# Optimization experiments

Measured on AMD Instinct MI355X. Metric: run time of the kernel, lower is better.

## Reference

```python
import jax, jax.numpy as jnp
import numpy as np

VOCAB = 50257
EXTRA = 64          # static over-approximation of num_oovs
SEQ = 1024
T_DEC = 100
E = 128
H = 160             # encoder hidden per direction; decoder hidden = 2H = 320
UNK = 3
START = 0
NEG = -1e9


def lstm_cell(x, h, c, wih, whh, bih, bhh):
    # torch gate order: i, f, g, o
    g = x @ wih.T + h @ whh.T + bih + bhh
    i, f, gg, o = jnp.split(g, 4, axis=-1)
    c = jax.nn.sigmoid(f) * c + jax.nn.sigmoid(i) * jnp.tanh(gg)
    h = jax.nn.sigmoid(o) * jnp.tanh(c)
    return h, c


def run_lstm(xs, wih, whh, bih, bhh, hdim):
    def step(carry, x):
        h, c = carry
        h, c = lstm_cell(x, h, c, wih, whh, bih, bhh)
        return (h, c), h
    init = (jnp.zeros((hdim,), xs.dtype), jnp.zeros((hdim,), xs.dtype))
    (hf, _), hs = jax.lax.scan(step, init, xs)
    return hs, hf


def setup_inputs() -> dict:
    key = jax.random.key(0)
    ks = jax.random.split(key, 20)
    rn = lambda k, shape, s: (jax.random.normal(k, shape, dtype=jnp.float32) * s)
    inp = {
        'input_ids': jax.random.randint(ks[0], (SEQ,), 0, VOCAB + EXTRA),
        'embedding': rn(ks[1], (VOCAB, E), 0.1),
        'enc_wih_f': rn(ks[2], (4 * H, E), 0.08),
        'enc_whh_f': rn(ks[3], (4 * H, H), 0.08),
        'enc_bih_f': rn(ks[4], (4 * H,), 0.05),
        'enc_bhh_f': rn(ks[5], (4 * H,), 0.05),
        'enc_wih_b': rn(ks[6], (4 * H, E), 0.08),
        'enc_whh_b': rn(ks[7], (4 * H, H), 0.08),
        'enc_bih_b': rn(ks[8], (4 * H,), 0.05),
        'enc_bhh_b': rn(ks[9], (4 * H,), 0.05),
        'dec_wih': rn(ks[10], (8 * H, E), 0.08),
        'dec_whh': rn(ks[11], (8 * H, 2 * H), 0.08),
        'dec_bih': rn(ks[12], (8 * H,), 0.05),
        'dec_bhh': rn(ks[13], (8 * H,), 0.05),
        'enc_attn_proj': rn(ks[14], (2 * H, 2 * H), 0.02),
        'dec_attn_proj': rn(ks[15], (2 * H, 2 * H), 0.02),
        'vocab_proj': rn(ks[16], (E, 6 * H), 0.05),
        'out_bias': rn(ks[17], (VOCAB,), 0.01),
        'switch_w': rn(ks[18], (1, 6 * H), 0.05),
        'switch_b': rn(ks[19], (1,), 0.05),
    }
    return inp


def reference(input_ids, embedding, enc_wih_f, enc_whh_f, enc_bih_f, enc_bhh_f,
              enc_wih_b, enc_whh_b, enc_bih_b, enc_bhh_b,
              dec_wih, dec_whh, dec_bih, dec_bhh,
              enc_attn_proj, dec_attn_proj, vocab_proj, out_bias,
              switch_w, switch_b):
    ids_in = jnp.where(input_ids >= VOCAB, UNK, input_ids)
    emb = embedding[ids_in]                               # [S, E]

    # bidirectional encoder LSTM
    h_fwd, hfin_f = run_lstm(emb, enc_wih_f, enc_whh_f, enc_bih_f, enc_bhh_f, H)
    h_bwd_rev, hfin_b = run_lstm(emb[::-1], enc_wih_b, enc_whh_b, enc_bih_b, enc_bhh_b, H)
    enc_h = jnp.concatenate([h_fwd, h_bwd_rev[::-1]], axis=-1)   # [S, 2H]

    # step-invariant vocab projection: tanh(W_emb @ vocab_proj) -> [V, 6H]
    out_proj = jnp.tanh(embedding @ vocab_proj)

    # precompute projected encoder states for attention: [S, 2H]
    enc_proj_h = enc_h @ enc_attn_proj.T

    h0 = jnp.concatenate([hfin_f, hfin_b])                # [2H]
    c0 = jnp.zeros((2 * H,), enc_h.dtype)
    dec_buf0 = jnp.zeros((T_DEC, 2 * H), enc_h.dtype)
    cum0 = jnp.zeros((SEQ,), enc_h.dtype)
    tok0 = jnp.asarray(START, dtype=input_ids.dtype)
    t_range = jnp.arange(T_DEC)

    def step(carry, t):
        h, c, cum, dec_buf, tok = carry
        x = embedding[jnp.where(tok >= VOCAB, UNK, tok)]
        h, c = lstm_cell(x, h, c, dec_wih, dec_whh, dec_bih, dec_bhh)

        # intra-temporal encoder attention
        scores = enc_proj_h @ h                           # [S] = h @ W_e @ enc_h.T
        cum_safe = jnp.where(t == 0, 1.0, cum)
        temporal = jnp.where(t == 0, scores, jnp.exp(scores) / cum_safe)
        attn = jax.nn.softmax(temporal)
        enc_ctx = attn @ enc_h                            # [2H]

        # intra-decoder attention over previous decoder hidden states
        dscores = (h @ dec_attn_proj) @ dec_buf.T         # [T_DEC]
        dmask = t_range < t
        dattn = jax.nn.softmax(jnp.where(dmask, dscores, NEG))
        dec_ctx = jnp.where(t == 0, jnp.zeros_like(h), dattn @ dec_buf)

        concat = jnp.concatenate([h, enc_ctx, dec_ctx])   # [6H]
        vocab_dist = jax.nn.softmax(out_proj @ concat + out_bias)  # [V]
        p_copy = jax.nn.sigmoid(jnp.dot(switch_w[0], concat) + switch_b[0])
        gen = jnp.pad((1.0 - p_copy) * vocab_dist, (0, EXTRA))     # [V+EXTRA]
        final = gen.at[input_ids].add(p_copy * attn)      # pointer scatter-add

        cum = cum + scores
        dec_buf = dec_buf.at[t].set(h)
        tok = jnp.argmax(final).astype(input_ids.dtype)   # greedy decode
        return (h, c, cum, dec_buf, tok), final

    _, finals = jax.lax.scan(step, (h0, c0, cum0, dec_buf0, tok0), t_range)
    return finals                                         # [T_DEC, V+EXTRA]
```

## Files before the change

### kernel.cpp

```cpp
#include <hip/hip_runtime.h>
#include <cstdint>

#define VOCAB 50257
#define VTOT  50321
#define TDEC  100
#define UNK   3
#define VPB   99

static const size_t OFF_EMB    = 0;
static const size_t OFF_WIHT_F = 131072;
static const size_t OFF_WIHT_B = 212992;
static const size_t OFF_WTE    = 294912;
static const size_t OFF_XG     = 397312;
static const size_t OFF_ENCH   = 1708032;
static const size_t OFF_EPH    = 2035712;
static const size_t OFF_DECBUF = 2363392;
static const size_t OFF_LOGITS = 2395392;
static const size_t OFF_SCORES = 2446080;
static const size_t OFF_GATES  = 2447104;
static const size_t OFF_HPAR   = 2448384;
static const size_t OFF_CPAR   = 2450944;
static const size_t OFF_DCTX   = 2456064;
static const size_t OFF_H      = 2456384;
static const size_t OFF_H0     = 2456704;
static const size_t OFF_CA     = 2457024;
static const size_t OFF_CB     = 2457344;
static const size_t OFF_CUMA   = 2457664;
static const size_t OFF_CUMB   = 2458688;
static const size_t OFF_ATTN   = 2459712;
static const size_t OFF_BM     = 2460736;
static const size_t OFF_BS     = 2461248;
static const size_t OFF_AVAL   = 2461760;
static const size_t OFF_AIDX   = 2462272;
static const size_t OFF_SCAL   = 2462784;
static const size_t OFF_SKEY   = 2462848;
static const size_t OFF_SPOS   = 2463872;
static const size_t OFF_BSTART = 2464896;
static const size_t OFF_WBF16  = 2465792;

__device__ __forceinline__ float sigmf(float x) { return 1.f / (1.f + expf(-x)); }

__device__ __forceinline__ float wsum64(float x) {
#pragma unroll
  for (int m = 1; m < 64; m <<= 1) x += __shfl_xor(x, m, 64);
  return x;
}

__device__ __forceinline__ unsigned short bf16r(float x) {
  uint32_t b = __float_as_uint(x);
  uint32_t r = (b + 0x7fffu + ((b >> 16) & 1u)) >> 16;
  return (unsigned short)r;
}

__global__ __launch_bounds__(256) void k_setup(float* __restrict__ ws, const int* __restrict__ ids,
                                               const float* __restrict__ embt, const float* __restrict__ ewf,
                                               const float* __restrict__ ewb, const float* __restrict__ eap) {
  int idx = blockIdx.x * 256 + threadIdx.x;
  if (idx < 131072) {
    int tt = idx >> 7, e = idx & 127;
    int id = ids[tt]; if (id >= VOCAB) id = UNK;
    ws[OFF_EMB + idx] = embt[(size_t)id * 128 + e];
  } else if (idx < 212992) {
    int i = idx - 131072;
    int k = i / 640, g = i - (i / 640) * 640;
    ws[OFF_WIHT_F + i] = ewf[(size_t)g * 128 + k];
  } else if (idx < 294912) {
    int i = idx - 212992;
    int k = i / 640, g = i - (i / 640) * 640;
    ws[OFF_WIHT_B + i] = ewb[(size_t)g * 128 + k];
  } else if (idx < 397312) {
    int i = idx - 294912;
    int k = i / 320, j = i - (i / 320) * 320;
    ws[OFF_WTE + i] = eap[(size_t)j * 320 + k];
  } else if (idx < 398656) {
    int i = idx - 397312;
    if (i < 320) ws[OFF_CA + i] = 0.f;
    else         ws[OFF_CUMA + (i - 320)] = 0.f;
  }
}

__global__ __launch_bounds__(256) void k_xg(float* __restrict__ ws,
                                            const float* __restrict__ bif, const float* __restrict__ bhf,
                                            const float* __restrict__ bib, const float* __restrict__ bhb) {
  int idx = blockIdx.x * 256 + threadIdx.x;
  int d = idx / 655360;
  int r = idx - d * 655360;
  int tt = r / 640, g = r - (r / 640) * 640;
  const float* wT = ws + (d ? OFF_WIHT_B : OFF_WIHT_F);
  const float* er = ws + OFF_EMB + (size_t)(d ? (1023 - tt) : tt) * 128;
  float acc = d ? (bib[g] + bhb[g]) : (bif[g] + bhf[g]);
#pragma unroll 4
  for (int k = 0; k < 128; ++k) acc += er[k] * wT[(size_t)k * 640 + g];
  ws[OFF_XG + idx] = acc;
}

__global__ __launch_bounds__(256) void k_outproj(const float* __restrict__ embt, const float* __restrict__ vp,
                                                 float* __restrict__ ws) {
  __shared__ float As[64][128];
  __shared__ float Bs[128][64];
  const int tid = threadIdx.x;
  const int v0 = blockIdx.x * 64, n0 = blockIdx.y * 64;
  for (int c = 0; c < 32; ++c) {
    int idx = c * 256 + tid;
    int m = idx >> 7, k = idx & 127;
    int v = v0 + m;
    As[m][k] = (v < VOCAB) ? embt[(size_t)v * 128 + k] : 0.f;
    int k2 = idx >> 6, n = idx & 63;
    Bs[k2][n] = vp[(size_t)k2 * 960 + n0 + n];
  }
  __syncthreads();
  const int mi = tid >> 4, ni = tid & 15;
  float acc[4][4] = {};
  for (int k = 0; k < 128; ++k) {
    float a0 = As[mi * 4 + 0][k], a1 = As[mi * 4 + 1][k], a2 = As[mi * 4 + 2][k], a3 = As[mi * 4 + 3][k];
    float4 b = *(const float4*)&Bs[k][ni * 4];
    acc[0][0] += a0 * b.x; acc[0][1] += a0 * b.y; acc[0][2] += a0 * b.z; acc[0][3] += a0 * b.w;
    acc[1][0] += a1 * b.x; acc[1][1] += a1 * b.y; acc[1][2] += a1 * b.z; acc[1][3] += a1 * b.w;
    acc[2][0] += a2 * b.x; acc[2][1] += a2 * b.y; acc[2][2] += a2 * b.z; acc[2][3] += a2 * b.w;
    acc[3][0] += a3 * b.x; acc[3][1] += a3 * b.y; acc[3][2] += a3 * b.z; acc[3][3] += a3 * b.w;
  }
  unsigned short* W = (unsigned short*)(ws + OFF_WBF16);
#pragma unroll
  for (int i = 0; i < 4; ++i) {
    int v = v0 + mi * 4 + i;
    if (v < VOCAB) {
      ushort4 pk;
      pk.x = bf16r(tanhf(acc[i][0]));
      pk.y = bf16r(tanhf(acc[i][1]));
      pk.z = bf16r(tanhf(acc[i][2]));
      pk.w = bf16r(tanhf(acc[i][3]));
      *(ushort4*)&W[(size_t)v * 960 + n0 + ni * 4] = pk;
    }
  }
}

__global__ __launch_bounds__(512) void k_encoder(float* __restrict__ ws, const float* __restrict__ whh_f,
                                                 const float* __restrict__ whh_b) {
  const int dir = blockIdx.x;
  const int tid = threadIdx.x;
  const float* whh = dir ? whh_b : whh_f;
  const float* xg = ws + OFF_XG + (size_t)dir * 655360;
  __shared__ float hbuf[160];
  __shared__ float part[4][640];
  const int q = tid & 127, kg = tid >> 7, ks = kg * 40;
  float w[5][40];
#pragma unroll
  for (int j = 0; j < 5; ++j)
#pragma unroll
    for (int i = 0; i < 40; ++i)
      w[j][i] = whh[(size_t)(5 * q + j) * 160 + ks + i];
  float cst = 0.f;
  if (tid < 160) hbuf[tid] = 0.f;
  __syncthreads();
  for (int t = 0; t < 1024; ++t) {
    float acc[5] = {0.f, 0.f, 0.f, 0.f, 0.f};
#pragma unroll
    for (int i4 = 0; i4 < 10; ++i4) {
      float4 h4 = *(const float4*)&hbuf[ks + i4 * 4];
#pragma unroll
      for (int j = 0; j < 5; ++j)
        acc[j] += w[j][i4 * 4 + 0] * h4.x + w[j][i4 * 4 + 1] * h4.y + w[j][i4 * 4 + 2] * h4.z + w[j][i4 * 4 + 3] * h4.w;
    }
#pragma unroll
    for (int j = 0; j < 5; ++j) part[kg][5 * q + j] = acc[j];
    __syncthreads();
    if (tid < 160) {
      float gi = xg[(size_t)t * 640 + tid];
      float gf = xg[(size_t)t * 640 + 160 + tid];
      float gg = xg[(size_t)t * 640 + 320 + tid];
      float go = xg[(size_t)t * 640 + 480 + tid];
#pragma unroll
      for (int k2 = 0; k2 < 4; ++k2) {
        gi += part[k2][tid]; gf += part[k2][160 + tid];
        gg += part[k2][320 + tid]; go += part[k2][480 + tid];
      }
      cst = sigmf(gf) * cst + sigmf(gi) * tanhf(gg);
      float hn = sigmf(go) * tanhf(cst);
      hbuf[tid] = hn;
      int trow = dir ? (1023 - t) : t;
      ws[OFF_ENCH + (size_t)trow * 320 + dir * 160 + tid] = hn;
    }
    __syncthreads();
  }
  if (tid < 160) ws[OFF_H0 + dir * 160 + tid] = hbuf[tid];
}

__global__ __launch_bounds__(256) void k_encproj(float* __restrict__ ws) {
  int idx = blockIdx.x * 256 + threadIdx.x;
  int s = idx / 320, j = idx - (idx / 320) * 320;
  const float* er = ws + OFF_ENCH + (size_t)s * 320;
  const float* wt = ws + OFF_WTE;
  float acc = 0.f;
#pragma unroll 4
  for (int k = 0; k < 320; ++k) acc += er[k] * wt[(size_t)k * 320 + j];
  ws[OFF_EPH + idx] = acc;
}

__global__ __launch_bounds__(512) void k_sort(float* __restrict__ ws, const int* __restrict__ ids) {
  __shared__ int sk[1024], sp[1024];
  const int tid = threadIdx.x;
  for (int j = tid; j < 1024; j += 512) { sk[j] = ids[j]; sp[j] = j; }
  if (tid < 320) ws[OFF_H + tid] = ws[OFF_H0 + tid];
  __syncthreads();
  for (int k = 2; k <= 1024; k <<= 1)
    for (int j = k >> 1; j > 0; j >>= 1) {
      for (int i = tid; i < 1024; i += 512) {
        int ixj = i ^ j;
        if (ixj > i) {
          bool up = ((i & k) == 0);
          int a = sk[i], b2 = sk[ixj];
          if (up ? (a > b2) : (a < b2)) {
            sk[i] = b2; sk[ixj] = a;
            int pa = sp[i]; sp[i] = sp[ixj]; sp[ixj] = pa;
          }
        }
      }
      __syncthreads();
    }
  int* BST = (int*)(ws + OFF_BSTART);
  int* SK = (int*)(ws + OFF_SKEY);
  int* SP = (int*)(ws + OFF_SPOS);
  for (int j = tid; j < 1024; j += 512) {
    SK[j] = sk[j]; SP[j] = sp[j];
    int o1 = sk[j] / VPB;
    int o0 = (j == 0) ? -1 : (sk[j - 1] / VPB);
    for (int o = o0 + 1; o <= o1; ++o) BST[o] = j;
  }
  if (tid == 0) {
    int olast = sk[1023] / VPB;
    for (int o = olast + 1; o <= 512; ++o) BST[o] = 1024;
  }
}

__global__ __launch_bounds__(256) void k_d1_gates(float* __restrict__ ws, const float* __restrict__ embt,
                                                  const float* __restrict__ dwih, const float* __restrict__ dwhh,
                                                  const float* __restrict__ dbih, const float* __restrict__ dbhh,
                                                  int t) {
  __shared__ float rv[256];
  __shared__ int ri[256];
  const int tid = threadIdx.x, bid = blockIdx.x;
  int token = 0;
  if (t > 0) {
    float v0 = ws[OFF_AVAL + tid], v1 = ws[OFF_AVAL + 256 + tid];
    int i0 = ((const int*)(ws + OFF_AIDX))[tid], i1 = ((const int*)(ws + OFF_AIDX))[256 + tid];
    if (v1 > v0 || (v1 == v0 && i1 < i0)) { v0 = v1; i0 = i1; }
    rv[tid] = v0; ri[tid] = i0;
    __syncthreads();
    for (int off = 128; off > 0; off >>= 1) {
      if (tid < off) {
        float b = rv[tid + off]; int bi = ri[tid + off];
        if (b > rv[tid] || (b == rv[tid] && bi < ri[tid])) { rv[tid] = b; ri[tid] = bi; }
      }
      __syncthreads();
    }
    token = ri[0];
  }
  int tokm = (token >= VOCAB) ? UNK : token;
  const int l = tid & 63, wv = tid >> 6;
  float xv0 = embt[(size_t)tokm * 128 + l];
  float xv1 = embt[(size_t)tokm * 128 + 64 + l];
  float hv[5];
#pragma unroll
  for (int c = 0; c < 5; ++c) hv[c] = ws[OFF_H + c * 64 + l];
  const int wg = bid * 4 + wv;
  for (int i = 0; i < 16; ++i) {
    const int r = wg * 16 + i;
    float acc = dwih[(size_t)r * 128 + l] * xv0 + dwih[(size_t)r * 128 + 64 + l] * xv1;
#pragma unroll
    for (int c = 0; c < 5; ++c) acc += dwhh[(size_t)r * 320 + c * 64 + l] * hv[c];
    acc = wsum64(acc);
    if (l == 0) ws[OFF_GATES + r] = acc + dbih[r] + dbhh[r];
  }
}

__global__ __launch_bounds__(512) void k_d2_hs(float* __restrict__ ws, const float* __restrict__ dap, int t) {
  __shared__ float hL[320];
  const int tid = threadIdx.x, bid = blockIdx.x;
  const int par = t & 1;
  const float* cin = ws + (par ? OFF_CB : OFF_CA);
  float* cout = ws + (par ? OFF_CA : OFF_CB);
  if (tid < 320) {
    float gi = ws[OFF_GATES + tid];
    float gf = ws[OFF_GATES + 320 + tid];
    float gg = ws[OFF_GATES + 640 + tid];
    float go = ws[OFF_GATES + 960 + tid];
    float c = sigmf(gf) * cin[tid] + sigmf(gi) * tanhf(gg);
    float hn = sigmf(go) * tanhf(c);
    hL[tid] = hn;
    if (bid == 0) {
      cout[tid] = c;
      ws[OFF_H + tid] = hn;
      ws[OFF_DECBUF + (size_t)t * 320 + tid] = hn;
    }
  }
  __syncthreads();
  if (bid < 32) {
    const int l = tid & 63, wv = tid >> 6;
    float hv[5];
#pragma unroll
    for (int c = 0; c < 5; ++c) hv[c] = hL[c * 64 + l];
#pragma unroll
    for (int i = 0; i < 4; ++i) {
      int s = bid * 32 + wv * 4 + i;
      const float* er = ws + OFF_EPH + (size_t)s * 320;
      float acc = 0.f;
#pragma unroll
      for (int c = 0; c < 5; ++c) acc += er[c * 64 + l] * hv[c];
      acc = wsum64(acc);
      if (l == 0) ws[OFF_SCORES + s] = acc;
    }
  } else if (tid < 320) {
    int q = bid - 32;
    float acc = 0.f;
#pragma unroll 8
    for (int ii = 0; ii < 40; ++ii) {
      int i = q * 40 + ii;
      acc += hL[i] * dap[(size_t)i * 320 + tid];
    }
    ws[OFF_HPAR + q * 320 + tid] = acc;
  }
}

__global__ __launch_bounds__(512) void k_d3_attn(float* __restrict__ ws, int t) {
  __shared__ float attnL[1024];
  __shared__ float redA[512];
  __shared__ float dsL[128];
  __shared__ float daL[128];
  __shared__ float hpL[320];
  const int tid = threadIdx.x, bid = blockIdx.x;
  const int par = t & 1;
  const float* cumin = ws + (par ? OFF_CUMB : OFF_CUMA);
  float* cumout = ws + (par ? OFF_CUMA : OFF_CUMB);

  if (bid < 16) {
    float s0 = ws[OFF_SCORES + tid];
    float s1 = ws[OFF_SCORES + 512 + tid];
    float t0 = (t == 0) ? s0 : expf(s0) / cumin[tid];
    float t1 = (t == 0) ? s1 : expf(s1) / cumin[512 + tid];
    redA[tid] = fmaxf(t0, t1);
    __syncthreads();
    for (int off = 256; off > 0; off >>= 1) { if (tid < off) redA[tid] = fmaxf(redA[tid], redA[tid + off]); __syncthreads(); }
    float mx = redA[0];
    __syncthreads();
    redA[tid] = expf(t0 - mx) + expf(t1 - mx);
    __syncthreads();
    for (int off = 256; off > 0; off >>= 1) { if (tid < off) redA[tid] += redA[tid + off]; __syncthreads(); }
    float Ssm = redA[0];
    __syncthreads();
    attnL[tid] = expf(t0 - mx) / Ssm;
    attnL[512 + tid] = expf(t1 - mx) / Ssm;
    __syncthreads();
    if (tid < 64) ws[OFF_ATTN + bid * 64 + tid] = attnL[bid * 64 + tid];
    if (tid < 320) {
      float acc = 0.f;
      const float* eh = ws + OFF_ENCH + (size_t)(bid * 64) * 320 + tid;
#pragma unroll 4
      for (int k2 = 0; k2 < 64; ++k2) acc += attnL[bid * 64 + k2] * eh[(size_t)k2 * 320];
      ws[OFF_CPAR + bid * 320 + tid] = acc;
    }
  } else {
    cumout[tid] = cumin[tid] + ws[OFF_SCORES + tid];
    cumout[512 + tid] = cumin[512 + tid] + ws[OFF_SCORES + 512 + tid];
    if (tid < 320) {
      float a = 0.f;
#pragma unroll
      for (int q = 0; q < 8; ++q) a += ws[OFF_HPAR + q * 320 + tid];
      hpL[tid] = a;
    }
    __syncthreads();
    const int l = tid & 63, wv = tid >> 6;
    float hpv[5];
#pragma unroll
    for (int c = 0; c < 5; ++c) hpv[c] = hpL[c * 64 + l];
#pragma unroll
    for (int k2 = 0; k2 < 13; ++k2) {
      int tp = wv + 8 * k2;
      if (tp < t) {
        float acc = 0.f;
#pragma unroll
        for (int c = 0; c < 5; ++c) acc += hpv[c] * ws[OFF_DECBUF + (size_t)tp * 320 + c * 64 + l];
        acc = wsum64(acc);
        if (l == 0) dsL[tp] = acc;
      }
    }
    __syncthreads();
    float dv = -1e30f;
    if (tid < 128) { dv = (tid < t) ? dsL[tid] : -1e30f; redA[tid] = dv; }
    __syncthreads();
    for (int off = 64; off > 0; off >>= 1) { if (tid < off) redA[tid] = fmaxf(redA[tid], redA[tid + off]); __syncthreads(); }
    float dmx = redA[0];
    __syncthreads();
    float de = (tid < 128) ? expf(dv - dmx) : 0.f;
    if (tid < 128) redA[tid] = de;
    __syncthreads();
    for (int off = 64; off > 0; off >>= 1) { if (tid < off) redA[tid] += redA[tid + off]; __syncthreads(); }
    float dS = redA[0];
    __syncthreads();
    if (tid < 128) daL[tid] = de / dS;
    __syncthreads();
    if (tid < 320) {
      float acc = 0.f;
      for (int tp = 0; tp < t; ++tp) acc += daL[tp] * ws[OFF_DECBUF + (size_t)tp * 320 + tid];
      ws[OFF_DCTX + tid] = acc;
    }
  }
}

__global__ __launch_bounds__(256) void k_d4_logits(float* __restrict__ ws, const float* __restrict__ ob,
                                                   const float* __restrict__ sw, const float* __restrict__ sb) {
  __shared__ float concatL[960];
  __shared__ float logitsL[128];
  __shared__ float rm[256], rs[256];
  const int tid = threadIdx.x, bid = blockIdx.x;
  for (int i = tid; i < 960; i += 256) {
    float v;
    if (i < 320) v = ws[OFF_H + i];
    else if (i < 640) {
      int j = i - 320;
      float a = 0.f;
#pragma unroll
      for (int p = 0; p < 16; ++p) a += ws[OFF_CPAR + p * 320 + j];
      v = a;
    } else v = ws[OFF_DCTX + (i - 640)];
    concatL[i] = v;
  }
  __syncthreads();
  const int l = tid & 63, wv = tid >> 6;
  if (bid == 0 && tid < 64) {
    float acc = 0.f;
#pragma unroll
    for (int c = 0; c < 15; ++c) acc += sw[c * 64 + l] * concatL[c * 64 + l];
    acc = wsum64(acc);
    if (l == 0) ws[OFF_SCAL] = 1.f / (1.f + expf(-(acc + sb[0])));
  }
  const unsigned* W = (const unsigned*)(ws + OFF_WBF16);
  const float2* cL2 = (const float2*)concatL;
  float cc0[7], cc1[7], ct0 = 0.f, ct1 = 0.f;
#pragma unroll
  for (int c = 0; c < 7; ++c) { float2 x = cL2[c * 64 + l]; cc0[c] = x.x; cc1[c] = x.y; }
  if (l < 32) { ct0 = concatL[896 + 2 * l]; ct1 = concatL[897 + 2 * l]; }
  const int vbase = bid * VPB;
  const int r0 = wv * 25, r1 = (wv * 25 + 25 < VPB) ? (wv * 25 + 25) : VPB;
  for (int r = r0; r < r1; r += 2) {
    int va = vbase + r, vb = va + 1;
    bool oka = (va < VOCAB);
    bool okb = (r + 1 < r1) && (vb < VOCAB);
    float acc0 = 0.f, acc1 = 0.f;
    const unsigned* rowa = W + (size_t)va * 480;
    const unsigned* rowb = W + (size_t)vb * 480;
    unsigned ua[7], ub[7], ta = 0, tb = 0;
    if (oka) {
#pragma unroll
      for (int c = 0; c < 7; ++c) ua[c] = rowa[c * 64 + l];
      if (l < 32) ta = rowa[448 + l];
    }
    if (okb) {
#pragma unroll
      for (int c = 0; c < 7; ++c) ub[c] = rowb[c * 64 + l];
      if (l < 32) tb = rowb[448 + l];
    }
    if (oka) {
#pragma unroll
      for (int c = 0; c < 7; ++c)
        acc0 += __uint_as_float(ua[c] << 16) * cc0[c] + __uint_as_float(ua[c] & 0xffff0000u) * cc1[c];
      if (l < 32) acc0 += __uint_as_float(ta << 16) * ct0 + __uint_as_float(ta & 0xffff0000u) * ct1;
    }
    if (okb) {
#pragma unroll
      for (int c = 0; c < 7; ++c)
        acc1 += __uint_as_float(ub[c] << 16) * cc0[c] + __uint_as_float(ub[c] & 0xffff0000u) * cc1[c];
      if (l < 32) acc1 += __uint_as_float(tb << 16) * ct0 + __uint_as_float(tb & 0xffff0000u) * ct1;
    }
    acc0 = wsum64(acc0);
    acc1 = wsum64(acc1);
    if (l == 0) {
      if (oka) { float lg = acc0 + ob[va]; logitsL[r] = lg; ws[OFF_LOGITS + va] = lg; }
      else logitsL[r] = -1e30f;
      if (r + 1 < r1) {
        if (okb) { float lg = acc1 + ob[vb]; logitsL[r + 1] = lg; ws[OFF_LOGITS + vb] = lg; }
        else logitsL[r + 1] = -1e30f;
      }
    }
  }
  __syncthreads();
  bool valid = (tid < VPB) && (logitsL[tid < VPB ? tid : 0] > -1e29f) && (tid < VPB);
  float m = -1e30f, s = 0.f;
  if (tid < VPB) {
    float lv = logitsL[tid];
    if (lv > -1e29f) { m = lv; s = 1.f; }
  }
  (void)valid;
  rm[tid] = m; rs[tid] = s;
  __syncthreads();
  for (int off = 128; off > 0; off >>= 1) {
    if (tid < off) {
      float m1 = rm[tid], m2 = rm[tid + off];
      float mm = fmaxf(m1, m2);
      rs[tid] = rs[tid] * expf(m1 - mm) + rs[tid + off] * expf(m2 - mm);
      rm[tid] = mm;
    }
    __syncthreads();
  }
  if (tid == 0) { ws[OFF_BM + bid] = rm[0]; ws[OFF_BS + bid] = rs[0]; }
}

__global__ __launch_bounds__(128) void k_d5_final(float* __restrict__ ws, float* __restrict__ out, int t) {
  __shared__ float rm[128], rs[128];
  __shared__ float rv[128];
  __shared__ int ri[128];
  const int tid = threadIdx.x, bid = blockIdx.x;
  float m = -1e30f, s = 0.f;
#pragma unroll
  for (int k = 0; k < 4; ++k) {
    float m2 = ws[OFF_BM + tid * 4 + k], s2 = ws[OFF_BS + tid * 4 + k];
    float mm = fmaxf(m, m2);
    s = s * expf(m - mm) + s2 * expf(m2 - mm);
    m = mm;
  }
  rm[tid] = m; rs[tid] = s;
  __syncthreads();
  for (int off = 64; off > 0; off >>= 1) {
    if (tid < off) {
      float m1 = rm[tid], m2 = rm[tid + off];
      float mm = fmaxf(m1, m2);
      rs[tid] = rs[tid] * expf(m1 - mm) + rs[tid + off] * expf(m2 - mm);
      rm[tid] = mm;
    }
    __syncthreads();
  }
  float M = rm[0], Sg = rs[0];
  float pc = ws[OFF_SCAL];
  float scale = (1.f - pc) / Sg;
  const int* BST = (const int*)(ws + OFF_BSTART);
  const int* SK = (const int*)(ws + OFF_SKEY);
  const int* SP = (const int*)(ws + OFF_SPOS);
  int v = bid * VPB + tid;
  bool act = (tid < VPB) && (v < VTOT);
  float val = -1e30f;
  if (act) {
    val = (v < VOCAB) ? scale * expf(ws[OFF_LOGITS + v] - M) : 0.f;
    int jb = BST[bid], je = BST[bid + 1];
    for (int j = jb; j < je; ++j)
      if (SK[j] == v) val += pc * ws[OFF_ATTN + SP[j]];
    out[(size_t)t * VTOT + v] = val;
  }
  rv[tid] = act ? val : -1e30f; ri[tid] = v;
  __syncthreads();
  for (int off = 64; off > 0; off >>= 1) {
    if (tid < off) {
      float v2 = rv[tid + off]; int i2 = ri[tid + off];
      if (v2 > rv[tid] || (v2 == rv[tid] && i2 < ri[tid])) { rv[tid] = v2; ri[tid] = i2; }
    }
    __syncthreads();
  }
  if (tid == 0) { ws[OFF_AVAL + bid] = rv[0]; ((int*)(ws + OFF_AIDX))[bid] = ri[0]; }
}

extern "C" void kernel_launch(void* const* d_in, const int* in_sizes, int n_in,
                              void* d_out, int out_size, void* d_ws, size_t ws_size,
                              hipStream_t stream) {
  const int*   ids  = (const int*)d_in[0];
  const float* embt = (const float*)d_in[1];
  const float* ewf  = (const float*)d_in[2];
  const float* ehf  = (const float*)d_in[3];
  const float* ebif = (const float*)d_in[4];
  const float* ebhf = (const float*)d_in[5];
  const float* ewb  = (const float*)d_in[6];
  const float* ehb  = (const float*)d_in[7];
  const float* ebib = (const float*)d_in[8];
  const float* ebhb = (const float*)d_in[9];
  const float* dwih = (const float*)d_in[10];
  const float* dwhh = (const float*)d_in[11];
  const float* dbih = (const float*)d_in[12];
  const float* dbhh = (const float*)d_in[13];
  const float* eap  = (const float*)d_in[14];
  const float* dap  = (const float*)d_in[15];
  const float* vp   = (const float*)d_in[16];
  const float* ob   = (const float*)d_in[17];
  const float* sw   = (const float*)d_in[18];
  const float* sb   = (const float*)d_in[19];
  float* out = (float*)d_out;
  float* ws  = (float*)d_ws;

  k_setup<<<1558, 256, 0, stream>>>(ws, ids, embt, ewf, ewb, eap);
  k_xg<<<5120, 256, 0, stream>>>(ws, ebif, ebhf, ebib, ebhb);
  k_outproj<<<dim3(786, 15), 256, 0, stream>>>(embt, vp, ws);
  k_encoder<<<2, 512, 0, stream>>>(ws, ehf, ehb);
  k_encproj<<<1280, 256, 0, stream>>>(ws);
  k_sort<<<1, 512, 0, stream>>>(ws, ids);

  for (int t = 0; t < TDEC; ++t) {
    k_d1_gates<<<20, 256, 0, stream>>>(ws, embt, dwih, dwhh, dbih, dbhh, t);
    k_d2_hs<<<40, 512, 0, stream>>>(ws, dap, t);
    k_d3_attn<<<17, 512, 0, stream>>>(ws, t);
    k_d4_logits<<<512, 256, 0, stream>>>(ws, ob, sw, sb);
    k_d5_final<<<512, 128, 0, stream>>>(ws, out, t);
  }
}
```

Measured before the change: 7.863 ms.

## Fuse per-step decoder kernels into one persistent kernel with grid barriers

```diff
diff --git a/kernel.cpp b/kernel.cpp
--- a/kernel.cpp
+++ b/kernel.cpp
@@ -5,7 +5,9 @@
 #define VTOT  50321
 #define TDEC  100
 #define UNK   3
-#define VPB   99
+#define NBLK  256
+#define NTHR  512
+#define VPB   198
 
 static const size_t OFF_EMB    = 0;
 static const size_t OFF_WIHT_F = 131072;
@@ -38,6 +40,10 @@
 static const size_t OFF_BSTART = 2464896;
 static const size_t OFF_WBF16  = 2465792;
 
+static const size_t OFF_PMS  = OFF_LOGITS;
+static const size_t OFF_TEMP = OFF_SCORES;
+static const size_t OFF_BAR  = OFF_SCAL;
+
 __device__ __forceinline__ float sigmf(float x) { return 1.f / (1.f + expf(-x)); }
 
 __device__ __forceinline__ float wsum64(float x) {
@@ -50,6 +56,25 @@
   uint32_t b = __float_as_uint(x);
   uint32_t r = (b + 0x7fffu + ((b >> 16) & 1u)) >> 16;
   return (unsigned short)r;
+}
+
+__device__ __forceinline__ void gridbar(float* ws) {
+  int* bar = (int*)(ws + OFF_BAR);
+  __syncthreads();
+  if (threadIdx.x == 0) {
+    __threadfence();
+    int g = __hip_atomic_load(&bar[1], __ATOMIC_RELAXED, __HIP_MEMORY_SCOPE_AGENT);
+    int old = __hip_atomic_fetch_add(&bar[0], 1, __ATOMIC_ACQ_REL, __HIP_MEMORY_SCOPE_AGENT);
+    if (old == NBLK - 1) {
+      __hip_atomic_store(&bar[0], 0, __ATOMIC_RELAXED, __HIP_MEMORY_SCOPE_AGENT);
+      __hip_atomic_store(&bar[1], g + 1, __ATOMIC_RELEASE, __HIP_MEMORY_SCOPE_AGENT);
+    } else {
+      while (__hip_atomic_load(&bar[1], __ATOMIC_RELAXED, __HIP_MEMORY_SCOPE_AGENT) == g)
+        __builtin_amdgcn_s_sleep(2);
+    }
+    __threadfence();
+  }
+  __syncthreads();
 }
 
 __global__ __launch_bounds__(256) void k_setup(float* __restrict__ ws, const int* __restrict__ ids,
@@ -72,10 +97,6 @@
     int i = idx - 294912;
     int k = i / 320, j = i - (i / 320) * 320;
     ws[OFF_WTE + i] = eap[(size_t)j * 320 + k];
-  } else if (idx < 398656) {
-    int i = idx - 397312;
-    if (i < 320) ws[OFF_CA + i] = 0.f;
-    else         ws[OFF_CUMA + (i - 320)] = 0.f;
   }
 }
 
@@ -200,7 +221,6 @@
   __shared__ int sk[1024], sp[1024];
   const int tid = threadIdx.x;
   for (int j = tid; j < 1024; j += 512) { sk[j] = ids[j]; sp[j] = j; }
-  if (tid < 320) ws[OFF_H + tid] = ws[OFF_H0 + tid];
   __syncthreads();
   for (int k = 2; k <= 1024; k <<= 1)
     for (int j = k >> 1; j > 0; j >>= 1) {
@@ -228,332 +248,306 @@
   }
   if (tid == 0) {
     int olast = sk[1023] / VPB;
-    for (int o = olast + 1; o <= 512; ++o) BST[o] = 1024;
-  }
-}
-
-__global__ __launch_bounds__(256) void k_d1_gates(float* __restrict__ ws, const float* __restrict__ embt,
-                                                  const float* __restrict__ dwih, const float* __restrict__ dwhh,
-                                                  const float* __restrict__ dbih, const float* __restrict__ dbhh,
-                                                  int t) {
-  __shared__ float rv[256];
-  __shared__ int ri[256];
-  const int tid = threadIdx.x, bid = blockIdx.x;
-  int token = 0;
-  if (t > 0) {
-    float v0 = ws[OFF_AVAL + tid], v1 = ws[OFF_AVAL + 256 + tid];
-    int i0 = ((const int*)(ws + OFF_AIDX))[tid], i1 = ((const int*)(ws + OFF_AIDX))[256 + tid];
-    if (v1 > v0 || (v1 == v0 && i1 < i0)) { v0 = v1; i0 = i1; }
-    rv[tid] = v0; ri[tid] = i0;
+    for (int o = olast + 1; o <= NBLK; ++o) BST[o] = 1024;
+    int* bar = (int*)(ws + OFF_BAR);
+    bar[0] = 0; bar[1] = 0;
+  }
+}
+
+__global__ __launch_bounds__(512) void k_decode(float* __restrict__ ws, float* __restrict__ out,
+    const float* __restrict__ embt,
+    const float* __restrict__ dwih, const float* __restrict__ dwhh,
+    const float* __restrict__ dbih, const float* __restrict__ dbhh,
+    const float* __restrict__ dap, const float* __restrict__ sw,
+    const float* __restrict__ sb, const float* __restrict__ ob) {
+  const int b = blockIdx.x, tid = threadIdx.x;
+  const int l = tid & 63, w = tid >> 6;
+  __shared__ float hL[320], cL[320];
+  __shared__ __align__(16) float concatL[960];
+  __shared__ float logitsL[VPB];
+  __shared__ float tauL[4], cumL[4];
+  __shared__ float redA[512], redB[512];
+  __shared__ int   redI[512];
+  __shared__ float attnL[64], dsL[128], daL[128], hpL[320];
+  __shared__ float pcS;
+
+  if (tid < 320) { hL[tid] = ws[OFF_H0 + tid]; cL[tid] = 0.f; }
+  if (tid < 4) cumL[tid] = 0.f;
+  __syncthreads();
+
+  for (int t = 0; t < TDEC; ++t) {
+    int token = 0;
+    if (t > 0) {
+      float av = -1e30f; int ai = 0;
+      if (tid < 256) { av = ws[OFF_AVAL + tid]; ai = ((const int*)(ws + OFF_AIDX))[tid]; }
+      redA[tid] = av; redI[tid] = ai;
+      __syncthreads();
+      for (int off = 256; off > 0; off >>= 1) {
+        if (tid < off) {
+          float v2 = redA[tid + off]; int i2 = redI[tid + off];
+          if (v2 > redA[tid] || (v2 == redA[tid] && i2 < redI[tid])) { redA[tid] = v2; redI[tid] = i2; }
+        }
+        __syncthreads();
+      }
+      token = redI[0];
+    }
+    int tokm = (token >= VOCAB) ? UNK : token;
+    if (w < 5) {
+      const int r = 5 * b + w;
+      float acc = dwih[(size_t)r * 128 + l] * embt[(size_t)tokm * 128 + l]
+                + dwih[(size_t)r * 128 + 64 + l] * embt[(size_t)tokm * 128 + 64 + l];
+#pragma unroll
+      for (int c = 0; c < 5; ++c) acc += dwhh[(size_t)r * 320 + c * 64 + l] * hL[c * 64 + l];
+      acc = wsum64(acc);
+      if (l == 0) ws[OFF_GATES + r] = acc + dbih[r] + dbhh[r];
+    }
+    gridbar(ws);
+
+    if (tid < 320) {
+      float gi = ws[OFF_GATES + tid];
+      float gf = ws[OFF_GATES + 320 + tid];
+      float gg = ws[OFF_GATES + 640 + tid];
+      float go = ws[OFF_GATES + 960 + tid];
+      float c = sigmf(gf) * cL[tid] + sigmf(gi) * tanhf(gg);
+      cL[tid] = c;
+      float hn = sigmf(go) * tanhf(c);
+      hL[tid] = hn;
+      if (b == 17) ws[OFF_DECBUF + (size_t)t * 320 + tid] = hn;
+    }
     __syncthreads();
-    for (int off = 128; off > 0; off >>= 1) {
-      if (tid < off) {
-        float b = rv[tid + off]; int bi = ri[tid + off];
-        if (b > rv[tid] || (b == rv[tid] && bi < ri[tid])) { rv[tid] = b; ri[tid] = bi; }
-      }
-      __syncthreads();
-    }
-    token = ri[0];
-  }
-  int tokm = (token >= VOCAB) ? UNK : token;
-  const int l = tid & 63, wv = tid >> 6;
-  float xv0 = embt[(size_t)tokm * 128 + l];
-  float xv1 = embt[(size_t)tokm * 128 + 64 + l];
-  float hv[5];
-#pragma unroll
-  for (int c = 0; c < 5; ++c) hv[c] = ws[OFF_H + c * 64 + l];
-  const int wg = bid * 4 + wv;
-  for (int i = 0; i < 16; ++i) {
-    const int r = wg * 16 + i;
-    float acc = dwih[(size_t)r * 128 + l] * xv0 + dwih[(size_t)r * 128 + 64 + l] * xv1;
-#pragma unroll
-    for (int c = 0; c < 5; ++c) acc += dwhh[(size_t)r * 320 + c * 64 + l] * hv[c];
-    acc = wsum64(acc);
-    if (l == 0) ws[OFF_GATES + r] = acc + dbih[r] + dbhh[r];
-  }
-}
-
-__global__ __launch_bounds__(512) void k_d2_hs(float* __restrict__ ws, const float* __restrict__ dap, int t) {
-  __shared__ float hL[320];
-  const int tid = threadIdx.x, bid = blockIdx.x;
-  const int par = t & 1;
-  const float* cin = ws + (par ? OFF_CB : OFF_CA);
-  float* cout = ws + (par ? OFF_CA : OFF_CB);
-  if (tid < 320) {
-    float gi = ws[OFF_GATES + tid];
-    float gf = ws[OFF_GATES + 320 + tid];
-    float gg = ws[OFF_GATES + 640 + tid];
-    float go = ws[OFF_GATES + 960 + tid];
-    float c = sigmf(gf) * cin[tid] + sigmf(gi) * tanhf(gg);
-    float hn = sigmf(go) * tanhf(c);
-    hL[tid] = hn;
-    if (bid == 0) {
-      cout[tid] = c;
-      ws[OFF_H + tid] = hn;
-      ws[OFF_DECBUF + (size_t)t * 320 + tid] = hn;
-    }
-  }
-  __syncthreads();
-  if (bid < 32) {
-    const int l = tid & 63, wv = tid >> 6;
-    float hv[5];
-#pragma unroll
-    for (int c = 0; c < 5; ++c) hv[c] = hL[c * 64 + l];
-#pragma unroll
-    for (int i = 0; i < 4; ++i) {
-      int s = bid * 32 + wv * 4 + i;
-      const float* er = ws + OFF_EPH + (size_t)s * 320;
+    if (w < 4) {
+      const int srow = 4 * b + w;
+      const float* er = ws + OFF_EPH + (size_t)srow * 320;
       float acc = 0.f;
 #pragma unroll
-      for (int c = 0; c < 5; ++c) acc += er[c * 64 + l] * hv[c];
+      for (int c = 0; c < 5; ++c) acc += er[c * 64 + l] * hL[c * 64 + l];
       acc = wsum64(acc);
-      if (l == 0) ws[OFF_SCORES + s] = acc;
-    }
-  } else if (tid < 320) {
-    int q = bid - 32;
-    float acc = 0.f;
+      float tau = (t == 0) ? acc : expf(acc) / cumL[w];
+      if (l == 0) {
+        tauL[w] = tau;
+        ws[OFF_TEMP + srow] = tau;
+        cumL[w] += acc;
+      }
+    }
+    if (b < 8 && tid < 320) {
+      float acc = 0.f;
 #pragma unroll 8
-    for (int ii = 0; ii < 40; ++ii) {
-      int i = q * 40 + ii;
-      acc += hL[i] * dap[(size_t)i * 320 + tid];
-    }
-    ws[OFF_HPAR + q * 320 + tid] = acc;
-  }
-}
-
-__global__ __launch_bounds__(512) void k_d3_attn(float* __restrict__ ws, int t) {
-  __shared__ float attnL[1024];
-  __shared__ float redA[512];
-  __shared__ float dsL[128];
-  __shared__ float daL[128];
-  __shared__ float hpL[320];
-  const int tid = threadIdx.x, bid = blockIdx.x;
-  const int par = t & 1;
-  const float* cumin = ws + (par ? OFF_CUMB : OFF_CUMA);
-  float* cumout = ws + (par ? OFF_CUMA : OFF_CUMB);
-
-  if (bid < 16) {
-    float s0 = ws[OFF_SCORES + tid];
-    float s1 = ws[OFF_SCORES + 512 + tid];
-    float t0 = (t == 0) ? s0 : expf(s0) / cumin[tid];
-    float t1 = (t == 0) ? s1 : expf(s1) / cumin[512 + tid];
-    redA[tid] = fmaxf(t0, t1);
+      for (int ii = 0; ii < 40; ++ii) {
+        int i = b * 40 + ii;
+        acc += hL[i] * dap[(size_t)i * 320 + tid];
+      }
+      ws[OFF_HPAR + b * 320 + tid] = acc;
+    }
     __syncthreads();
-    for (int off = 256; off > 0; off >>= 1) { if (tid < off) redA[tid] = fmaxf(redA[tid], redA[tid + off]); __syncthreads(); }
-    float mx = redA[0];
+    if (tid == 0) {
+      float m4 = fmaxf(fmaxf(tauL[0], tauL[1]), fmaxf(tauL[2], tauL[3]));
+      float s4 = expf(tauL[0] - m4) + expf(tauL[1] - m4) + expf(tauL[2] - m4) + expf(tauL[3] - m4);
+      ws[OFF_PMS + 2 * b] = m4;
+      ws[OFF_PMS + 2 * b + 1] = s4;
+    }
+    gridbar(ws);
+
+    if (b < 16) {
+      float m = -1e30f, s = 0.f;
+      if (tid < 256) { m = ws[OFF_PMS + 2 * tid]; s = ws[OFF_PMS + 2 * tid + 1]; }
+      redA[tid] = m; redB[tid] = s;
+      __syncthreads();
+      for (int off = 256; off > 0; off >>= 1) {
+        if (tid < off) {
+          float m1 = redA[tid], m2 = redA[tid + off];
+          float mx = fmaxf(m1, m2);
+          redB[tid] = redB[tid] * expf(m1 - mx) + redB[tid + off] * expf(m2 - mx);
+          redA[tid] = mx;
+        }
+        __syncthreads();
+      }
+      const float M = redA[0], S = redB[0];
+      __syncthreads();
+      if (tid < 64) {
+        float a = expf(ws[OFF_TEMP + 64 * b + tid] - M) / S;
+        attnL[tid] = a;
+        ws[OFF_ATTN + 64 * b + tid] = a;
+      }
+      __syncthreads();
+      if (tid < 320) {
+        float acc = 0.f;
+        const float* eh = ws + OFF_ENCH + (size_t)(64 * b) * 320 + tid;
+#pragma unroll 4
+        for (int k2 = 0; k2 < 64; ++k2) acc += attnL[k2] * eh[(size_t)k2 * 320];
+        ws[OFF_CPAR + b * 320 + tid] = acc;
+      }
+    } else if (b == 16) {
+      if (tid < 320) {
+        float a = 0.f;
+#pragma unroll
+        for (int q = 0; q < 8; ++q) a += ws[OFF_HPAR + q * 320 + tid];
+        hpL[tid] = a;
+      }
+      __syncthreads();
+      float hpv[5];
+#pragma unroll
+      for (int c = 0; c < 5; ++c) hpv[c] = hpL[c * 64 + l];
+#pragma unroll
+      for (int k2 = 0; k2 < 13; ++k2) {
+        int tp = w + 8 * k2;
+        if (tp < t) {
+          float acc = 0.f;
+#pragma unroll
+          for (int c = 0; c < 5; ++c) acc += hpv[c] * ws[OFF_DECBUF + (size_t)tp * 320 + c * 64 + l];
+          acc = wsum64(acc);
+          if (l == 0) dsL[tp] = acc;
+        }
+      }
+      __syncthreads();
+      float dv = -1e30f;
+      if (tid < 128) { dv = (tid < t) ? dsL[tid] : -1e30f; redA[tid] = dv; }
+      __syncthreads();
+      for (int off = 64; off > 0; off >>= 1) { if (tid < off) redA[tid] = fmaxf(redA[tid], redA[tid + off]); __syncthreads(); }
+      float dmx = redA[0];
+      __syncthreads();
+      float de = (tid < 128) ? expf(dv - dmx) : 0.f;
+      if (tid < 128) redA[tid] = de;
+      __syncthreads();
+      for (int off = 64; off > 0; off >>= 1) { if (tid < off) redA[tid] += redA[tid + off]; __syncthreads(); }
+      float dS = redA[0];
+      __syncthreads();
+      if (tid < 128) daL[tid] = de / dS;
+      __syncthreads();
+      if (tid < 320) {
+        float acc = 0.f;
+        for (int tp = 0; tp < t; ++tp) acc += daL[tp] * ws[OFF_DECBUF + (size_t)tp * 320 + tid];
+        ws[OFF_DCTX + tid] = (t == 0) ? 0.f : acc;
+      }
+    }
+    gridbar(ws);
+
+    if (tid < 320) {
+      float e = 0.f;
+#pragma unroll
+      for (int g2 = 0; g2 < 16; ++g2) e += ws[OFF_CPAR + g2 * 320 + tid];
+      concatL[tid] = hL[tid];
+      concatL[320 + tid] = e;
+      concatL[640 + tid] = ws[OFF_DCTX + tid];
+    }
     __syncthreads();
-    redA[tid] = expf(t0 - mx) + expf(t1 - mx);
+    if (w == 0) {
+      float acc = 0.f;
+#pragma unroll
+      for (int c = 0; c < 15; ++c) acc += sw[c * 64 + l] * concatL[c * 64 + l];
+      acc = wsum64(acc);
+      if (l == 0) pcS = 1.f / (1.f + expf(-(acc + sb[0])));
+    }
+    {
+      const unsigned* W = (const unsigned*)(ws + OFF_WBF16);
+      const float2* cL2 = (const float2*)concatL;
+      float cc0[7], cc1[7], ct0 = 0.f, ct1 = 0.f;
+#pragma unroll
+      for (int c = 0; c < 7; ++c) { float2 x = cL2[c * 64 + l]; cc0[c] = x.x; cc1[c] = x.y; }
+      if (l < 32) { ct0 = concatL[896 + 2 * l]; ct1 = concatL[897 + 2 * l]; }
+      const int vbase = b * VPB;
+      const int r0 = w * 25, r1 = (w * 25 + 25 < VPB) ? (w * 25 + 25) : VPB;
+      for (int r = r0; r < r1; r += 2) {
+        int va = vbase + r, vb2 = va + 1;
+        bool oka = (va < VOCAB);
+        bool okb = (r + 1 < r1) && (vb2 < VOCAB);
+        float acc0 = 0.f, acc1 = 0.f;
+        const unsigned* rowa = W + (size_t)va * 480;
+        const unsigned* rowb = W + (size_t)vb2 * 480;
+        unsigned ua[7], ub[7], ta = 0, tb = 0;
+        if (oka) {
+#pragma unroll
+          for (int c = 0; c < 7; ++c) ua[c] = rowa[c * 64 + l];
+          if (l < 32) ta = rowa[448 + l];
+        }
+        if (okb) {
+#pragma unroll
+          for (int c = 0; c < 7; ++c) ub[c] = rowb[c * 64 + l];
+          if (l < 32) tb = rowb[448 + l];
+        }
+        if (oka) {
+#pragma unroll
+          for (int c = 0; c < 7; ++c)
+            acc0 += __uint_as_float(ua[c] << 16) * cc0[c] + __uint_as_float(ua[c] & 0xffff0000u) * cc1[c];
+          if (l < 32) acc0 += __uint_as_float(ta << 16) * ct0 + __uint_as_float(ta & 0xffff0000u) * ct1;
+        }
+        if (okb) {
+#pragma unroll
+          for (int c = 0; c < 7; ++c)
+            acc1 += __uint_as_float(ub[c] << 16) * cc0[c] + __uint_as_float(ub[c] & 0xffff0000u) * cc1[c];
+          if (l < 32) acc1 += __uint_as_float(tb << 16) * ct0 + __uint_as_float(tb & 0xffff0000u) * ct1;
+        }
+        acc0 = wsum64(acc0);
+        acc1 = wsum64(acc1);
+        if (l == 0) {
+          logitsL[r] = oka ? (acc0 + ob[va]) : -1e30f;
+          if (r + 1 < r1) logitsL[r + 1] = okb ? (acc1 + ob[vb2]) : -1e30f;
+        }
+      }
+    }
     __syncthreads();
-    for (int off = 256; off > 0; off >>= 1) { if (tid < off) redA[tid] += redA[tid + off]; __syncthreads(); }
-    float Ssm = redA[0];
-    __syncthreads();
-    attnL[tid] = expf(t0 - mx) / Ssm;
-    attnL[512 + tid] = expf(t1 - mx) / Ssm;
-    __syncthreads();
-    if (tid < 64) ws[OFF_ATTN + bid * 64 + tid] = attnL[bid * 64 + tid];
-    if (tid < 320) {
-      float acc = 0.f;
-      const float* eh = ws + OFF_ENCH + (size_t)(bid * 64) * 320 + tid;
-#pragma unroll 4
-      for (int k2 = 0; k2 < 64; ++k2) acc += attnL[bid * 64 + k2] * eh[(size_t)k2 * 320];
-      ws[OFF_CPAR + bid * 320 + tid] = acc;
-    }
-  } else {
-    cumout[tid] = cumin[tid] + ws[OFF_SCORES + tid];
-    cumout[512 + tid] = cumin[512 + tid] + ws[OFF_SCORES + 512 + tid];
-    if (tid < 320) {
-      float a = 0.f;
-#pragma unroll
-      for (int q = 0; q < 8; ++q) a += ws[OFF_HPAR + q * 320 + tid];
-      hpL[tid] = a;
-    }
-    __syncthreads();
-    const int l = tid & 63, wv = tid >> 6;
-    float hpv[5];
-#pragma unroll
-    for (int c = 0; c < 5; ++c) hpv[c] = hpL[c * 64 + l];
-#pragma unroll
-    for (int k2 = 0; k2 < 13; ++k2) {
-      int tp = wv + 8 * k2;
-      if (tp < t) {
-        float acc = 0.f;
-#pragma unroll
-        for (int c = 0; c < 5; ++c) acc += hpv[c] * ws[OFF_DECBUF + (size_t)tp * 320 + c * 64 + l];
-        acc = wsum64(acc);
-        if (l == 0) dsL[tp] = acc;
-      }
-    }
-    __syncthreads();
-    float dv = -1e30f;
-    if (tid < 128) { dv = (tid < t) ? dsL[tid] : -1e30f; redA[tid] = dv; }
-    __syncthreads();
-    for (int off = 64; off > 0; off >>= 1) { if (tid < off) redA[tid] = fmaxf(redA[tid], redA[tid + off]); __syncthreads(); }
-    float dmx = redA[0];
-    __syncthreads();
-    float de = (tid < 128) ? expf(dv - dmx) : 0.f;
-    if (tid < 128) redA[tid] = de;
-    __syncthreads();
-    for (int off = 64; off > 0; off >>= 1) { if (tid < off) redA[tid] += redA[tid + off]; __syncthreads(); }
-    float dS = redA[0];
-    __syncthreads();
-    if (tid < 128) daL[tid] = de / dS;
-    __syncthreads();
-    if (tid < 320) {
-      float acc = 0.f;
-      for (int tp = 0; tp < t; ++tp) acc += daL[tp] * ws[OFF_DECBUF + (size_t)tp * 320 + tid];
-      ws[OFF_DCTX + tid] = acc;
-    }
-  }
-}
-
-__global__ __launch_bounds__(256) void k_d4_logits(float* __restrict__ ws, const float* __restrict__ ob,
-                                                   const float* __restrict__ sw, const float* __restrict__ sb) {
-  __shared__ float concatL[960];
-  __shared__ float logitsL[128];
-  __shared__ float rm[256], rs[256];
-  const int tid = threadIdx.x, bid = blockIdx.x;
-  for (int i = tid; i < 960; i += 256) {
-    float v;
-    if (i < 320) v = ws[OFF_H + i];
-    else if (i < 640) {
-      int j = i - 320;
-      float a = 0.f;
-#pragma unroll
-      for (int p = 0; p < 16; ++p) a += ws[OFF_CPAR + p * 320 + j];
-      v = a;
-    } else v = ws[OFF_DCTX + (i - 640)];
-    concatL[i] = v;
-  }
-  __syncthreads();
-  const int l = tid & 63, wv = tid >> 6;
-  if (bid == 0 && tid < 64) {
-    float acc = 0.f;
-#pragma unroll
-    for (int c = 0; c < 15; ++c) acc += sw[c * 64 + l] * concatL[c * 64 + l];
-    acc = wsum64(acc);
-    if (l == 0) ws[OFF_SCAL] = 1.f / (1.f + expf(-(acc + sb[0])));
-  }
-  const unsigned* W = (const unsigned*)(ws + OFF_WBF16);
-  const float2* cL2 = (const float2*)concatL;
-  float cc0[7], cc1[7], ct0 = 0.f, ct1 = 0.f;
-#pragma unroll
-  for (int c = 0; c < 7; ++c) { float2 x = cL2[c * 64 + l]; cc0[c] = x.x; cc1[c] = x.y; }
-  if (l < 32) { ct0 = concatL[896 + 2 * l]; ct1 = concatL[897 + 2 * l]; }
-  const int vbase = bid * VPB;
-  const int r0 = wv * 25, r1 = (wv * 25 + 25 < VPB) ? (wv * 25 + 25) : VPB;
-  for (int r = r0; r < r1; r += 2) {
-    int va = vbase + r, vb = va + 1;
-    bool oka = (va < VOCAB);
-    bool okb = (r + 1 < r1) && (vb < VOCAB);
-    float acc0 = 0.f, acc1 = 0.f;
-    const unsigned* rowa = W + (size_t)va * 480;
-    const unsigned* rowb = W + (size_t)vb * 480;
-    unsigned ua[7], ub[7], ta = 0, tb = 0;
-    if (oka) {
-#pragma unroll
-      for (int c = 0; c < 7; ++c) ua[c] = rowa[c * 64 + l];
-      if (l < 32) ta = rowa[448 + l];
-    }
-    if (okb) {
-#pragma unroll
-      for (int c = 0; c < 7; ++c) ub[c] = rowb[c * 64 + l];
-      if (l < 32) tb = rowb[448 + l];
-    }
-    if (oka) {
-#pragma unroll
-      for (int c = 0; c < 7; ++c)
-        acc0 += __uint_as_float(ua[c] << 16) * cc0[c] + __uint_as_float(ua[c] & 0xffff0000u) * cc1[c];
-      if (l < 32) acc0 += __uint_as_float(ta << 16) * ct0 + __uint_as_float(ta & 0xffff0000u) * ct1;
-    }
-    if (okb) {
-#pragma unroll
-      for (int c = 0; c < 7; ++c)
-        acc1 += __uint_as_float(ub[c] << 16) * cc0[c] + __uint_as_float(ub[c] & 0xffff0000u) * cc1[c];
-      if (l < 32) acc1 += __uint_as_float(tb << 16) * ct0 + __uint_as_float(tb & 0xffff0000u) * ct1;
-    }
-    acc0 = wsum64(acc0);
-    acc1 = wsum64(acc1);
-    if (l == 0) {
-      if (oka) { float lg = acc0 + ob[va]; logitsL[r] = lg; ws[OFF_LOGITS + va] = lg; }
-      else logitsL[r] = -1e30f;
-      if (r + 1 < r1) {
-        if (okb) { float lg = acc1 + ob[vb]; logitsL[r + 1] = lg; ws[OFF_LOGITS + vb] = lg; }
-        else logitsL[r + 1] = -1e30f;
-      }
-    }
-  }
-  __syncthreads();
-  bool valid = (tid < VPB) && (logitsL[tid < VPB ? tid : 0] > -1e29f) && (tid < VPB);
-  float m = -1e30f, s = 0.f;
-  if (tid < VPB) {
-    float lv = logitsL[tid];
-    if (lv > -1e29f) { m = lv; s = 1.f; }
-  }
-  (void)valid;
-  rm[tid] = m; rs[tid] = s;
-  __syncthreads();
-  for (int off = 128; off > 0; off >>= 1) {
-    if (tid < off) {
-      float m1 = rm[tid], m2 = rm[tid + off];
-      float mm = fmaxf(m1, m2);
-      rs[tid] = rs[tid] * expf(m1 - mm) + rs[tid + off] * expf(m2 - mm);
-      rm[tid] = mm;
-    }
-    __syncthreads();
-  }
-  if (tid == 0) { ws[OFF_BM + bid] = rm[0]; ws[OFF_BS + bid] = rs[0]; }
-}
-
-__global__ __launch_bounds__(128) void k_d5_final(float* __restrict__ ws, float* __restrict__ out, int t) {
-  __shared__ float rm[128], rs[128];
-  __shared__ float rv[128];
-  __shared__ int ri[128];
-  const int tid = threadIdx.x, bid = blockIdx.x;
-  float m = -1e30f, s = 0.f;
-#pragma unroll
-  for (int k = 0; k < 4; ++k) {
-    float m2 = ws[OFF_BM + tid * 4 + k], s2 = ws[OFF_BS + tid * 4 + k];
-    float mm = fmaxf(m, m2);
-    s = s * expf(m - mm) + s2 * expf(m2 - mm);
-    m = mm;
-  }
-  rm[tid] = m; rs[tid] = s;
-  __syncthreads();
-  for (int off = 64; off > 0; off >>= 1) {
-    if (tid < off) {
-      float m1 = rm[tid], m2 = rm[tid + off];
-      float mm = fmaxf(m1, m2);
-      rs[tid] = rs[tid] * expf(m1 - mm) + rs[tid + off] * expf(m2 - mm);
-      rm[tid] = mm;
-    }
-    __syncthreads();
-  }
-  float M = rm[0], Sg = rs[0];
-  float pc = ws[OFF_SCAL];
-  float scale = (1.f - pc) / Sg;
-  const int* BST = (const int*)(ws + OFF_BSTART);
-  const int* SK = (const int*)(ws + OFF_SKEY);
-  const int* SP = (const int*)(ws + OFF_SPOS);
-  int v = bid * VPB + tid;
-  bool act = (tid < VPB) && (v < VTOT);
-  float val = -1e30f;
-  if (act) {
-    val = (v < VOCAB) ? scale * expf(ws[OFF_LOGITS + v] - M) : 0.f;
-    int jb = BST[bid], je = BST[bid + 1];
-    for (int j = jb; j < je; ++j)
-      if (SK[j] == v) val += pc * ws[OFF_ATTN + SP[j]];
-    out[(size_t)t * VTOT + v] = val;
-  }
-  rv[tid] = act ? val : -1e30f; ri[tid] = v;
-  __syncthreads();
-  for (int off = 64; off > 0; off >>= 1) {
-    if (tid < off) {
-      float v2 = rv[tid + off]; int i2 = ri[tid + off];
-      if (v2 > rv[tid] || (v2 == rv[tid] && i2 < ri[tid])) { rv[tid] = v2; ri[tid] = i2; }
-    }
-    __syncthreads();
-  }
-  if (tid == 0) { ws[OFF_AVAL + bid] = rv[0]; ((int*)(ws + OFF_AIDX))[bid] = ri[0]; }
+    {
+      float m = -1e30f, s = 0.f;
+      if (tid < VPB) { float lv = logitsL[tid]; if (lv > -1e29f) { m = lv; s = 1.f; } }
+      redA[tid] = m; redB[tid] = s;
+      __syncthreads();
+      for (int off = 256; off > 0; off >>= 1) {
+        if (tid < off) {
+          float m1 = redA[tid], m2 = redA[tid + off];
+          float mx = fmaxf(m1, m2);
+          redB[tid] = redB[tid] * expf(m1 - mx) + redB[tid + off] * expf(m2 - mx);
+          redA[tid] = mx;
+        }
+        __syncthreads();
+      }
+      if (tid == 0) { ws[OFF_BM + b] = redA[0]; ws[OFF_BS + b] = redB[0]; }
+    }
+    gridbar(ws);
+
+    {
+      float m = -1e30f, s = 0.f;
+      if (tid < 256) { m = ws[OFF_BM + tid]; s = ws[OFF_BS + tid]; }
+      redA[tid] = m; redB[tid] = s;
+      __syncthreads();
+      for (int off = 256; off > 0; off >>= 1) {
+        if (tid < off) {
+          float m1 = redA[tid], m2 = redA[tid + off];
+          float mx = fmaxf(m1, m2);
+          redB[tid] = redB[tid] * expf(m1 - mx) + redB[tid + off] * expf(m2 - mx);
+          redA[tid] = mx;
+        }
+        __syncthreads();
+      }
+      const float M = redA[0], Sg = redB[0];
+      const float pc = pcS;
+      const float scale = (1.f - pc) / Sg;
+      __syncthreads();
+      const int* BST = (const int*)(ws + OFF_BSTART);
+      const int* SK = (const int*)(ws + OFF_SKEY);
+      const int* SP = (const int*)(ws + OFF_SPOS);
+      const int vbase = b * VPB;
+      int v = vbase + tid;
+      bool act = (tid < VPB) && (v < VTOT);
+      float val = -1e30f;
+      if (act) {
+        val = (v < VOCAB) ? scale * expf(logitsL[tid] - M) : 0.f;
+        int jb = BST[b], je = BST[b + 1];
+        for (int j = jb; j < je; ++j)
+          if (SK[j] == v) val += pc * ws[OFF_ATTN + SP[j]];
+        out[(size_t)t * VTOT + v] = val;
+      }
+      redA[tid] = act ? val : -1e30f; redI[tid] = v;
+      __syncthreads();
+      for (int off = 256; off > 0; off >>= 1) {
+        if (tid < off) {
+          float v2 = redA[tid + off]; int i2 = redI[tid + off];
+          if (v2 > redA[tid] || (v2 == redA[tid] && i2 < redI[tid])) { redA[tid] = v2; redI[tid] = i2; }
+        }
+        __syncthreads();
+      }
+      if (tid == 0) { ws[OFF_AVAL + b] = redA[0]; ((int*)(ws + OFF_AIDX))[b] = redI[0]; }
+    }
+    gridbar(ws);
+  }
 }
 
 extern "C" void kernel_launch(void* const* d_in, const int* in_sizes, int n_in,
@@ -588,12 +582,5 @@
   k_encoder<<<2, 512, 0, stream>>>(ws, ehf, ehb);
   k_encproj<<<1280, 256, 0, stream>>>(ws);
   k_sort<<<1, 512, 0, stream>>>(ws, ids);
-
-  for (int t = 0; t < TDEC; ++t) {
-    k_d1_gates<<<20, 256, 0, stream>>>(ws, embt, dwih, dwhh, dbih, dbhh, t);
-    k_d2_hs<<<40, 512, 0, stream>>>(ws, dap, t);
-    k_d3_attn<<<17, 512, 0, stream>>>(ws, t);
-    k_d4_logits<<<512, 256, 0, stream>>>(ws, ob, sw, sb);
-    k_d5_final<<<512, 128, 0, stream>>>(ws, out, t);
-  }
-}
+  k_decode<<<NBLK, NTHR, 0, stream>>>(ws, out, embt, dwih, dwhh, dbih, dbhh, dap, sw, sb, ob);
+}
```

Result: slower. 17.10 ms (+117.4%).
